# Kernel optimization log

Hardware: AMD Instinct MI355X
Metric: run time of the kernel (lower is better)

The kernel has to match this reference:

```python
import jax, jax.numpy as jnp
import numpy as np

EMBED_DIM = 4096
N_HEADS = 32
N_KV_HEADS = N_HEADS // 2
HEAD_DIM = EMBED_DIM // N_HEADS
MAX_SEQ_LEN = 4096


def setup_inputs() -> dict:
    key = jax.random.key(0)
    k1, k2, k3, k4, k5 = jax.random.split(key, 5)
    b, s = 1, 2048
    x = jax.random.normal(k1, (b, s, EMBED_DIM), dtype=jnp.float32)
    # rotary frequencies: theta=10000, angles[t, i] = t * 10000^{-2i/head_dim}
    inv_freq = 1.0 / (10000.0 ** (np.arange(0, HEAD_DIM, 2, dtype=np.float32) / HEAD_DIM))
    t = np.arange(MAX_SEQ_LEN, dtype=np.float32)
    ang = np.outer(t, inv_freq)  # [max_seq, head_dim/2]
    freqs_cis = jnp.asarray(np.stack([np.cos(ang), np.sin(ang)], axis=-1))  # [max_seq, hd/2, 2]
    scale = 0.02
    wq = jax.random.normal(k2, (EMBED_DIM, EMBED_DIM), dtype=jnp.float32) * scale
    wk = jax.random.normal(k3, (EMBED_DIM, N_KV_HEADS * HEAD_DIM), dtype=jnp.float32) * scale
    wv = jax.random.normal(k4, (EMBED_DIM, N_KV_HEADS * HEAD_DIM), dtype=jnp.float32) * scale
    wo = jax.random.normal(k5, (EMBED_DIM, EMBED_DIM), dtype=jnp.float32) * scale
    return {"x": x, "freqs_cis": freqs_cis, "wq": wq, "wk": wk, "wv": wv, "wo": wo, "start_pos": 0}


def _apply_rope(t, cos, sin):
    # t: [b, s, h, hd]; cos/sin: [1, s, 1, hd/2]
    tr = t.reshape(*t.shape[:-1], HEAD_DIM // 2, 2)
    t0, t1 = tr[..., 0], tr[..., 1]
    o0 = t0 * cos - t1 * sin
    o1 = t0 * sin + t1 * cos
    return jnp.stack([o0, o1], axis=-1).reshape(t.shape)


def reference(x, freqs_cis, wq, wk, wv, wo, start_pos):
    b, s, _ = x.shape
    q = (x @ wq).reshape(b, s, N_HEADS, HEAD_DIM)
    k = (x @ wk).reshape(b, s, N_KV_HEADS, HEAD_DIM)
    v = (x @ wv).reshape(b, s, N_KV_HEADS, HEAD_DIM)
    rep = N_HEADS // N_KV_HEADS
    k = jnp.repeat(k, rep, axis=2)  # GQA: expand KV heads (matches repeat_interleave)
    v = jnp.repeat(v, rep, axis=2)
    fc = freqs_cis[start_pos:start_pos + s]  # [s, hd/2, 2]
    cos = fc[None, :, None, :, 0]
    sin = fc[None, :, None, :, 1]
    q = _apply_rope(q, cos, sin)
    k = _apply_rope(k, cos, sin)
    # [b, h, s, hd]
    q = q.transpose(0, 2, 1, 3)
    k = k.transpose(0, 2, 1, 3)
    v = v.transpose(0, 2, 1, 3)
    scale = 1.0 / jnp.sqrt(jnp.float32(HEAD_DIM))
    scores = jnp.einsum("bhqd,bhkd->bhqk", q, k) * scale
    causal = jnp.tril(jnp.ones((s, s), dtype=bool))
    scores = jnp.where(causal[None, None], scores, jnp.finfo(scores.dtype).min)
    probs = jax.nn.softmax(scores, axis=-1)
    out = jnp.einsum("bhqk,bhkd->bhqd", probs, v)
    out = out.transpose(0, 2, 1, 3).reshape(b, s, EMBED_DIM)
    return out @ wo
```

## Files before the change

### kernel.cpp

```cpp
#include <hip/hip_runtime.h>
#include <stdint.h>

typedef unsigned short u16;
typedef __bf16 bf16x8 __attribute__((ext_vector_type(8)));
typedef float f32x4 __attribute__((ext_vector_type(4)));

#define SEQ   2048
#define EMBED 4096
#define KDIM  4096
#define NH    32
#define NKV   16
#define HD    128
#define KVW   2048

__device__ __forceinline__ float bf2f(u16 u) {
  union { uint32_t u; float f; } v; v.u = ((uint32_t)u) << 16; return v.f;
}
__device__ __forceinline__ u16 f2bf(float f) {
  union { float f; uint32_t u; } v; v.f = f;
  return (u16)((v.u + 0x7FFFu + ((v.u >> 16) & 1u)) >> 16);
}
__device__ __forceinline__ void g2l16(const u16* g, u16* l) {
  __builtin_amdgcn_global_load_lds(
      (const __attribute__((address_space(1))) uint32_t*)g,
      (__attribute__((address_space(3))) uint32_t*)l, 16, 0, 0);
}

__global__ __launch_bounds__(256) void convert_x(
    const float* __restrict__ X, u16* __restrict__ Xb, int nquad) {
  for (int i = blockIdx.x * 256 + threadIdx.x; i < nquad;
       i += gridDim.x * 256) {
    float4 v = *(const float4*)(X + (size_t)i * 4);
    ushort4 o;
    o.x = f2bf(v.x); o.y = f2bf(v.y); o.z = f2bf(v.z); o.w = f2bf(v.w);
    *(ushort4*)(Xb + (size_t)i * 4) = o;
  }
}

__global__ __launch_bounds__(256) void transpose_cvt(
    const float* __restrict__ W, u16* __restrict__ Wt, int K, int N) {
  __shared__ u16 tile[64][68];
  const int t = threadIdx.x;
  const int n0 = blockIdx.x * 64, k0 = blockIdx.y * 64;
#pragma unroll
  for (int i = 0; i < 4; i++) {
    int c = i * 256 + t;
    int r = c >> 4, cq = c & 15;
    float4 v = *(const float4*)(W + (size_t)(k0 + r) * N + n0 + cq * 4);
    tile[r][cq * 4 + 0] = f2bf(v.x); tile[r][cq * 4 + 1] = f2bf(v.y);
    tile[r][cq * 4 + 2] = f2bf(v.z); tile[r][cq * 4 + 3] = f2bf(v.w);
  }
  __syncthreads();
#pragma unroll
  for (int i = 0; i < 4; i++) {
    int c = i * 256 + t;
    int rn = c >> 4, cq = c & 15;
    ushort4 v;
    v.x = tile[cq * 4 + 0][rn];
    v.y = tile[cq * 4 + 1][rn];
    v.z = tile[cq * 4 + 2][rn];
    v.w = tile[cq * 4 + 3][rn];
    *(ushort4*)(Wt + (size_t)(n0 + rn) * K + k0 + cq * 4) = v;
  }
}

__global__ __launch_bounds__(512, 2) void gemm8_qkv(
    const u16* __restrict__ A,
    const u16* __restrict__ B0, const u16* __restrict__ B1,
    const u16* __restrict__ B2,
    u16* __restrict__ Qo, u16* __restrict__ Ko, u16* __restrict__ Vt) {
  __shared__ __align__(16) u16 As[2][256 * 64];
  __shared__ __align__(16) u16 Bs[2][256 * 64];
  const int t = threadIdx.x;
  const int lane = t & 63;
  const int w = t >> 6;
  const int wr = w >> 2;
  const int wc = w & 3;
  const int g = lane >> 4;
  const int l15 = lane & 15;

  const int bid = blockIdx.x;
  const int swz = (bid & 7) * 32 + (bid >> 3);
  const int mb = swz & 7;
  const int nb = swz >> 3;
  const int m0 = mb * 256;

  const u16* Bt; int nrow0;
  if (nb < 16)      { Bt = B0; nrow0 = nb * 256; }
  else if (nb < 24) { Bt = B1; nrow0 = (nb - 16) * 256; }
  else              { Bt = B2; nrow0 = (nb - 24) * 256; }

  auto stageA = [&](int buf, int kt, int h) {
#pragma unroll
    for (int i = 0; i < 2; i++) {
      int c = i * 512 + t;
      int row = c >> 3, sp = c & 7;
      int col = (sp ^ (row & 7)) << 3;
      g2l16(A + (size_t)(m0 + h * 128 + row) * KDIM + kt + col,
            &As[buf][h * 8192 + c * 8]);
    }
  };
  auto stageB = [&](int buf, int kt, int h) {
#pragma unroll
    for (int i = 0; i < 2; i++) {
      int c = i * 512 + t;
      int row = c >> 3, sp = c & 7;
      int col = (sp ^ (row & 7)) << 3;
      g2l16(Bt + (size_t)(nrow0 + h * 128 + row) * KDIM + kt + col,
            &Bs[buf][h * 8192 + c * 8]);
    }
  };

  f32x4 acc[8][4];
#pragma unroll
  for (int i = 0; i < 8; i++)
#pragma unroll
    for (int j = 0; j < 4; j++) acc[i][j] = (f32x4){0.f, 0.f, 0.f, 0.f};

  stageA(0, 0, 0); stageA(0, 0, 1);
  stageB(0, 0, 0); stageB(0, 0, 1);
  stageA(1, 64, 0); stageA(1, 64, 1);
  stageB(1, 64, 0); stageB(1, 64, 1);
  asm volatile("s_waitcnt vmcnt(8)" ::: "memory");
  __builtin_amdgcn_s_barrier();

  const int NT = KDIM / 64;
  for (int ti = 0; ti < NT; ++ti) {
    const int cur = ti & 1;
    const u16* Asc = As[cur];
    const u16* Bsc = Bs[cur];
    const int ktn2 = (ti + 2) * 64;
    bf16x8 a0[2][4], a1[2][4], b0[2][2], b1[2][2];

#pragma unroll
    for (int kk = 0; kk < 2; kk++)
#pragma unroll
      for (int mi = 0; mi < 4; mi++) {
        int r = wr * 128 + mi * 16 + l15;
        int slot = (kk * 4 + g) ^ (r & 7);
        a0[kk][mi] = *(const bf16x8*)(Asc + r * 64 + slot * 8);
      }
#pragma unroll
    for (int kk = 0; kk < 2; kk++)
#pragma unroll
      for (int ni = 0; ni < 2; ni++) {
        int r = wc * 64 + ni * 16 + l15;
        int slot = (kk * 4 + g) ^ (r & 7);
        b0[kk][ni] = *(const bf16x8*)(Bsc + r * 64 + slot * 8);
      }
    __builtin_amdgcn_s_barrier();
    asm volatile("s_waitcnt lgkmcnt(0)" ::: "memory");
    __builtin_amdgcn_sched_barrier(0);
    __builtin_amdgcn_s_setprio(1);
#pragma unroll
    for (int mi = 0; mi < 4; mi++)
#pragma unroll
      for (int ni = 0; ni < 2; ni++)
#pragma unroll
        for (int kk = 0; kk < 2; kk++)
          acc[mi][ni] = __builtin_amdgcn_mfma_f32_16x16x32_bf16(
              a0[kk][mi], b0[kk][ni], acc[mi][ni], 0, 0, 0);
    __builtin_amdgcn_s_setprio(0);
    __builtin_amdgcn_s_barrier();

#pragma unroll
    for (int kk = 0; kk < 2; kk++)
#pragma unroll
      for (int mi = 0; mi < 4; mi++) {
        int r = wr * 128 + 64 + mi * 16 + l15;
        int slot = (kk * 4 + g) ^ (r & 7);
        a1[kk][mi] = *(const bf16x8*)(Asc + r * 64 + slot * 8);
      }
    __builtin_amdgcn_s_barrier();
    asm volatile("s_waitcnt lgkmcnt(0)" ::: "memory");
    __builtin_amdgcn_sched_barrier(0);
    __builtin_amdgcn_s_setprio(1);
#pragma unroll
    for (int mi = 0; mi < 4; mi++)
#pragma unroll
      for (int ni = 0; ni < 2; ni++)
#pragma unroll
        for (int kk = 0; kk < 2; kk++)
          acc[mi + 4][ni] = __builtin_amdgcn_mfma_f32_16x16x32_bf16(
              a1[kk][mi], b0[kk][ni], acc[mi + 4][ni], 0, 0, 0);
    __builtin_amdgcn_s_setprio(0);
    __builtin_amdgcn_s_barrier();

#pragma unroll
    for (int kk = 0; kk < 2; kk++)
#pragma unroll
      for (int ni = 0; ni < 2; ni++) {
        int r = wc * 64 + (ni + 2) * 16 + l15;
        int slot = (kk * 4 + g) ^ (r & 7);
        b1[kk][ni] = *(const bf16x8*)(Bsc + r * 64 + slot * 8);
      }
    if (ti + 2 < NT) { stageA(cur, ktn2, 0); stageA(cur, ktn2, 1); }
    __builtin_amdgcn_s_barrier();
    asm volatile("s_waitcnt lgkmcnt(0)" ::: "memory");
    __builtin_amdgcn_sched_barrier(0);
    __builtin_amdgcn_s_setprio(1);
#pragma unroll
    for (int mi = 0; mi < 4; mi++)
#pragma unroll
      for (int ni = 0; ni < 2; ni++)
#pragma unroll
        for (int kk = 0; kk < 2; kk++)
          acc[mi + 4][ni + 2] = __builtin_amdgcn_mfma_f32_16x16x32_bf16(
              a1[kk][mi], b1[kk][ni], acc[mi + 4][ni + 2], 0, 0, 0);
    __builtin_amdgcn_s_setprio(0);
    __builtin_amdgcn_s_barrier();

    if (ti + 2 < NT) { stageB(cur, ktn2, 0); stageB(cur, ktn2, 1); }
    __builtin_amdgcn_s_barrier();
    __builtin_amdgcn_s_setprio(1);
#pragma unroll
    for (int mi = 0; mi < 4; mi++)
#pragma unroll
      for (int ni = 0; ni < 2; ni++)
#pragma unroll
        for (int kk = 0; kk < 2; kk++)
          acc[mi][ni + 2] = __builtin_amdgcn_mfma_f32_16x16x32_bf16(
              a0[kk][mi], b1[kk][ni], acc[mi][ni + 2], 0, 0, 0);
    __builtin_amdgcn_s_setprio(0);
    if (ti + 2 < NT)      asm volatile("s_waitcnt vmcnt(8)" ::: "memory");
    else if (ti + 1 < NT) asm volatile("s_waitcnt vmcnt(0)" ::: "memory");
    __builtin_amdgcn_s_barrier();
  }

#pragma unroll
  for (int mi = 0; mi < 8; mi++) {
#pragma unroll
    for (int ni = 0; ni < 4; ni++) {
      int rowg = m0 + wr * 128 + mi * 16 + g * 4;
      int ncol = nb * 256 + wc * 64 + ni * 16 + l15;
      if (nb < 16) {
#pragma unroll
        for (int r = 0; r < 4; r++)
          Qo[(size_t)(rowg + r) * EMBED + ncol] = f2bf(acc[mi][ni][r]);
      } else if (nb < 24) {
        int nc = ncol - 4096;
#pragma unroll
        for (int r = 0; r < 4; r++)
          Ko[(size_t)(rowg + r) * KVW + nc] = f2bf(acc[mi][ni][r]);
      } else {
        int nc = ncol - 6144;
        ushort4 v;
        v.x = f2bf(acc[mi][ni][0]); v.y = f2bf(acc[mi][ni][1]);
        v.z = f2bf(acc[mi][ni][2]); v.w = f2bf(acc[mi][ni][3]);
        *(ushort4*)(Vt + (size_t)nc * SEQ + rowg) = v;
      }
    }
  }
}

__global__ __launch_bounds__(512, 2) void gemm8_op(
    const u16* __restrict__ A, const u16* __restrict__ Bt,
    float* __restrict__ Cf) {
  __shared__ __align__(16) u16 As[2][128 * 64];
  __shared__ __align__(16) u16 Bs[2][256 * 64];
  const int t = threadIdx.x;
  const int lane = t & 63;
  const int w = t >> 6;
  const int wr = w >> 2;
  const int wc = w & 3;
  const int g = lane >> 4;
  const int l15 = lane & 15;

  const int bid = blockIdx.x;
  const int swz = (bid & 7) * 32 + (bid >> 3);
  const int mb = swz & 15;
  const int nb = swz >> 4;
  const int m0 = mb * 128;
  const int nrow0 = nb * 256;

  auto stageA = [&](int buf, int kt) {
#pragma unroll
    for (int i = 0; i < 2; i++) {
      int c = i * 512 + t;
      int row = c >> 3, sp = c & 7;
      int col = (sp ^ (row & 7)) << 3;
      g2l16(A + (size_t)(m0 + row) * KDIM + kt + col, &As[buf][c * 8]);
    }
  };
  auto stageB = [&](int buf, int kt) {
#pragma unroll
    for (int i = 0; i < 4; i++) {
      int c = i * 512 + t;
      int row = c >> 3, sp = c & 7;
      int col = (sp ^ (row & 7)) << 3;
      g2l16(Bt + (size_t)(nrow0 + row) * KDIM + kt + col, &Bs[buf][c * 8]);
    }
  };

  f32x4 acc[4][4];
#pragma unroll
  for (int i = 0; i < 4; i++)
#pragma unroll
    for (int j = 0; j < 4; j++) acc[i][j] = (f32x4){0.f, 0.f, 0.f, 0.f};

  stageA(0, 0); stageB(0, 0);
  stageA(1, 64); stageB(1, 64);
  asm volatile("s_waitcnt vmcnt(6)" ::: "memory");
  __builtin_amdgcn_s_barrier();

  const int NT = KDIM / 64;
  for (int ti = 0; ti < NT; ++ti) {
    const int cur = ti & 1;
    const u16* Asc = As[cur];
    const u16* Bsc = Bs[cur];
    const int ktn2 = (ti + 2) * 64;
    bf16x8 a[2][4], b0[2][2], b1[2][2];

#pragma unroll
    for (int kk = 0; kk < 2; kk++)
#pragma unroll
      for (int mi = 0; mi < 4; mi++) {
        int r = wr * 64 + mi * 16 + l15;
        int slot = (kk * 4 + g) ^ (r & 7);
        a[kk][mi] = *(const bf16x8*)(Asc + r * 64 + slot * 8);
      }
#pragma unroll
    for (int kk = 0; kk < 2; kk++)
#pragma unroll
      for (int ni = 0; ni < 2; ni++) {
        int r = wc * 64 + ni * 16 + l15;
        int slot = (kk * 4 + g) ^ (r & 7);
        b0[kk][ni] = *(const bf16x8*)(Bsc + r * 64 + slot * 8);
      }
#pragma unroll
    for (int kk = 0; kk < 2; kk++)
#pragma unroll
      for (int ni = 0; ni < 2; ni++) {
        int r = wc * 64 + (ni + 2) * 16 + l15;
        int slot = (kk * 4 + g) ^ (r & 7);
        b1[kk][ni] = *(const bf16x8*)(Bsc + r * 64 + slot * 8);
      }
    __builtin_amdgcn_s_barrier();
    asm volatile("s_waitcnt lgkmcnt(0)" ::: "memory");
    __builtin_amdgcn_sched_barrier(0);
    __builtin_amdgcn_s_setprio(1);
#pragma unroll
    for (int mi = 0; mi < 4; mi++)
#pragma unroll
      for (int ni = 0; ni < 2; ni++)
#pragma unroll
        for (int kk = 0; kk < 2; kk++)
          acc[mi][ni] = __builtin_amdgcn_mfma_f32_16x16x32_bf16(
              a[kk][mi], b0[kk][ni], acc[mi][ni], 0, 0, 0);
    __builtin_amdgcn_s_setprio(0);
    __builtin_amdgcn_s_barrier();

    if (ti + 2 < NT) { stageA(cur, ktn2); stageB(cur, ktn2); }
    __builtin_amdgcn_s_barrier();
    __builtin_amdgcn_s_setprio(1);
#pragma unroll
    for (int mi = 0; mi < 4; mi++)
#pragma unroll
      for (int ni = 0; ni < 2; ni++)
#pragma unroll
        for (int kk = 0; kk < 2; kk++)
          acc[mi][ni + 2] = __builtin_amdgcn_mfma_f32_16x16x32_bf16(
              a[kk][mi], b1[kk][ni], acc[mi][ni + 2], 0, 0, 0);
    __builtin_amdgcn_s_setprio(0);
    if (ti + 2 < NT)      asm volatile("s_waitcnt vmcnt(6)" ::: "memory");
    else if (ti + 1 < NT) asm volatile("s_waitcnt vmcnt(0)" ::: "memory");
    __builtin_amdgcn_s_barrier();
  }

#pragma unroll
  for (int mi = 0; mi < 4; mi++)
#pragma unroll
    for (int ni = 0; ni < 4; ni++) {
      int rowg = m0 + wr * 64 + mi * 16 + g * 4;
      int ncol = nb * 256 + wc * 64 + ni * 16 + l15;
#pragma unroll
      for (int r = 0; r < 4; r++)
        Cf[(size_t)(rowg + r) * 4096 + ncol] = acc[mi][ni][r];
    }
}

__global__ __launch_bounds__(256) void rope_kernel(
    u16* __restrict__ Q, u16* __restrict__ Kb,
    const float* __restrict__ freqs, const int* __restrict__ start_pos) {
  const int sp = start_pos[0];
  const float qscale = 0.08838834764831845f;
  const int total_q = SEQ * EMBED / 2;
  const int total_k = SEQ * KVW / 2;
  const int total = total_q + total_k;
  for (int idx = blockIdx.x * 256 + threadIdx.x; idx < total;
       idx += gridDim.x * 256) {
    u16* buf; int row, pi; bool isq = idx < total_q;
    if (isq) { row = idx >> 11; pi = idx & 2047; buf = Q + (size_t)row * EMBED; }
    else { int j = idx - total_q; row = j >> 10; pi = j & 1023; buf = Kb + (size_t)row * KVW; }
    int i = pi & 63;
    float2 cs = *(const float2*)(freqs + (size_t)(sp + row) * 128 + i * 2);
    float c = cs.x, s = cs.y;
    ushort2 tv = *(ushort2*)(buf + pi * 2);
    float t0 = bf2f(tv.x), t1 = bf2f(tv.y);
    float o0 = t0 * c - t1 * s;
    float o1 = t0 * s + t1 * c;
    if (isq) { o0 *= qscale; o1 *= qscale; }
    ushort2 o; o.x = f2bf(o0); o.y = f2bf(o1);
    *(ushort2*)(buf + pi * 2) = o;
  }
}

__global__ __launch_bounds__(256, 4) void attn_kernel(
    const u16* __restrict__ Q, const u16* __restrict__ Kb,
    const u16* __restrict__ Vt, u16* __restrict__ O) {
  __shared__ __align__(16) u16 KV[16384];
  __shared__ u16 Ps[4][16 * 72];

  const int t = threadIdx.x;
  const int lane = t & 63;
  const int w = t >> 6;
  const int g = lane >> 4;
  const int l15 = lane & 15;
  const int bid = blockIdx.x;
  const int qb = 31 - (bid >> 5);
  const int h = bid & 31;
  const int hk = h >> 1;

  auto stageK = [&](int kv) {
#pragma unroll
    for (int i = 0; i < 4; i++) {
      int c = i * 256 + t;
      int row = c >> 4, spp = c & 15;
      int col = ((spp ^ (row & 7)) << 3);
      g2l16(Kb + (size_t)(kv * 64 + row) * KVW + hk * HD + col, &KV[c * 8]);
    }
  };
  auto stageV = [&](int kv) {
#pragma unroll
    for (int i = 0; i < 4; i++) {
      int c = i * 256 + t;
      int row = c >> 3, spp = c & 7;
      int col = ((spp ^ (row & 7)) << 3);
      g2l16(Vt + (size_t)(hk * HD + row) * SEQ + kv * 64 + col,
            &KV[8192 + c * 8]);
    }
  };

#pragma unroll
  for (int i = 0; i < 4; i++) {
    int c = i * 256 + t;
    int row = c >> 4, spp = c & 15;
    int col = ((spp ^ (row & 7)) << 3);
    g2l16(Q + (size_t)(qb * 64 + row) * EMBED + h * HD + col, &KV[c * 8]);
  }
  asm volatile("s_waitcnt vmcnt(0)" ::: "memory");
  __builtin_amdgcn_s_barrier();

  bf16x8 qf[4];
  {
    int r = w * 16 + l15;
#pragma unroll
    for (int kk = 0; kk < 4; kk++) {
      int ps = (kk * 4 + g) ^ (r & 7);
      qf[kk] = *(const bf16x8*)(&KV[r * 128 + ps * 8]);
    }
  }
  asm volatile("s_waitcnt lgkmcnt(0)" ::: "memory");
  __builtin_amdgcn_s_barrier();

  f32x4 oacc[8];
#pragma unroll
  for (int i = 0; i < 8; i++) oacc[i] = (f32x4){0.f, 0.f, 0.f, 0.f};
  float mrow = -1e30f, lrow = 0.f;
  const int qg = qb * 64 + w * 16 + l15;

  for (int kv = 0; kv <= qb; kv++) {
    stageK(kv); stageV(kv);
    asm volatile("s_waitcnt vmcnt(0)" ::: "memory");
    __builtin_amdgcn_s_barrier();

    f32x4 sfragT[4];
    __builtin_amdgcn_s_setprio(1);
#pragma unroll
    for (int ni = 0; ni < 4; ni++) {
      f32x4 s = (f32x4){0.f, 0.f, 0.f, 0.f};
      int r = ni * 16 + l15;
#pragma unroll
      for (int kk = 0; kk < 4; kk++) {
        int ps = (kk * 4 + g) ^ (r & 7);
        bf16x8 a = *(const bf16x8*)(&KV[r * 128 + ps * 8]);
        s = __builtin_amdgcn_mfma_f32_16x16x32_bf16(a, qf[kk], s, 0, 0, 0);
      }
      sfragT[ni] = s;
    }
    __builtin_amdgcn_s_setprio(0);

    if (kv == qb) {
#pragma unroll
      for (int ni = 0; ni < 4; ni++) {
        int colg = kv * 64 + ni * 16 + g * 4;
#pragma unroll
        for (int r = 0; r < 4; r++)
          if (colg + r > qg) sfragT[ni][r] = -1e30f;
      }
    }

    float m16 = sfragT[0][0];
#pragma unroll
    for (int ni = 0; ni < 4; ni++)
#pragma unroll
      for (int r = 0; r < 4; r++) m16 = fmaxf(m16, sfragT[ni][r]);
    m16 = fmaxf(m16, __shfl_xor(m16, 16));
    m16 = fmaxf(m16, __shfl_xor(m16, 32));
    float mnew = fmaxf(mrow, m16);
    float sc = __expf(mrow - mnew);
    mrow = mnew;

    float rsum = 0.f;
#pragma unroll
    for (int ni = 0; ni < 4; ni++) {
#pragma unroll
      for (int r = 0; r < 4; r++) {
        float p = __expf(sfragT[ni][r] - mrow);
        rsum += p;
        Ps[w][l15 * 72 + ni * 16 + g * 4 + r] = f2bf(p);
      }
    }
    rsum += __shfl_xor(rsum, 16);
    rsum += __shfl_xor(rsum, 32);
    lrow = lrow * sc + rsum;

    float scr[4];
#pragma unroll
    for (int r = 0; r < 4; r++) scr[r] = __shfl(sc, g * 4 + r, 64);
#pragma unroll
    for (int nf = 0; nf < 8; nf++)
#pragma unroll
      for (int r = 0; r < 4; r++) oacc[nf][r] *= scr[r];

    asm volatile("s_waitcnt lgkmcnt(0)" ::: "memory");

    bf16x8 pa[2];
#pragma unroll
    for (int kk = 0; kk < 2; kk++)
      pa[kk] = *(const bf16x8*)(&Ps[w][l15 * 72 + kk * 32 + g * 8]);
    __builtin_amdgcn_s_setprio(1);
#pragma unroll
    for (int nf = 0; nf < 8; nf++) {
      int r = nf * 16 + l15;
#pragma unroll
      for (int kk = 0; kk < 2; kk++) {
        int ps = (kk * 4 + g) ^ (r & 7);
        bf16x8 b = *(const bf16x8*)(&KV[8192 + r * 64 + ps * 8]);
        oacc[nf] = __builtin_amdgcn_mfma_f32_16x16x32_bf16(pa[kk], b, oacc[nf], 0, 0, 0);
      }
    }
    __builtin_amdgcn_s_setprio(0);
    __builtin_amdgcn_s_barrier();
  }

  float lr[4];
#pragma unroll
  for (int r = 0; r < 4; r++) lr[r] = __shfl(lrow, g * 4 + r, 64);
#pragma unroll
  for (int nf = 0; nf < 8; nf++) {
#pragma unroll
    for (int r = 0; r < 4; r++) {
      int rowg = qb * 64 + w * 16 + g * 4 + r;
      float v = oacc[nf][r] / lr[r];
      O[(size_t)rowg * EMBED + h * HD + nf * 16 + l15] = f2bf(v);
    }
  }
}

extern "C" void kernel_launch(void* const* d_in, const int* in_sizes, int n_in,
                              void* d_out, int out_size, void* d_ws, size_t ws_size,
                              hipStream_t stream) {
  const float* x  = (const float*)d_in[0];
  const float* fc = (const float*)d_in[1];
  const float* wq = (const float*)d_in[2];
  const float* wk = (const float*)d_in[3];
  const float* wv = (const float*)d_in[4];
  const float* wo = (const float*)d_in[5];
  const int* sp = (const int*)d_in[6];

  char* ws = (char*)d_ws;
  u16* wqT = (u16*)(ws);
  u16* wkT = (u16*)(ws + 33554432ull);
  u16* wvT = (u16*)(ws + 50331648ull);
  u16* woT = (u16*)(ws + 67108864ull);
  u16* xb  = (u16*)(ws + 100663296ull);
  u16* Qb  = (u16*)(ws + 117440512ull);
  u16* Kb  = (u16*)(ws + 134217728ull);
  u16* Vt  = (u16*)(ws + 142606336ull);
  u16* Ob  = (u16*)(ws + 150994944ull);

  convert_x<<<dim3(2048), 256, 0, stream>>>(x, xb, SEQ * EMBED / 4);
  transpose_cvt<<<dim3(64, 64), 256, 0, stream>>>(wq, wqT, 4096, 4096);
  transpose_cvt<<<dim3(32, 64), 256, 0, stream>>>(wk, wkT, 4096, 2048);
  transpose_cvt<<<dim3(32, 64), 256, 0, stream>>>(wv, wvT, 4096, 2048);
  transpose_cvt<<<dim3(64, 64), 256, 0, stream>>>(wo, woT, 4096, 4096);

  gemm8_qkv<<<dim3(256), 512, 0, stream>>>(xb, wqT, wkT, wvT, Qb, Kb, Vt);
  rope_kernel<<<dim3(2048), 256, 0, stream>>>(Qb, Kb, fc, sp);
  attn_kernel<<<dim3(1024), 256, 0, stream>>>(Qb, Kb, Vt, Ob);
  gemm8_op<<<dim3(256), 512, 0, stream>>>(Ob, woT, (float*)d_out);
}
```

Baseline: 360.5 us.

## Software-pipeline LDS fragment reads across k-tiles in QKV and output GEMMs

Restructures the main loops of both GEMM kernels so the first A/B fragments for the next k-tile are read from LDS while MFMAs of the current tile run, with ping-pong register sets and a loop unrolled by two. It removes several barriers and lgkmcnt waits per iteration and interleaves global-to-LDS staging with fragment reads and MFMA blocks. This should hide LDS latency and cut sync overhead. In exchange it raises register pressure and relies on tighter vmcnt counts for correctness.

```diff
diff --git a/kernel.cpp b/kernel.cpp
--- a/kernel.cpp
+++ b/kernel.cpp
@@ -24,6 +24,11 @@
   __builtin_amdgcn_global_load_lds(
       (const __attribute__((address_space(1))) uint32_t*)g,
       (__attribute__((address_space(3))) uint32_t*)l, 16, 0, 0);
+}
+__device__ __forceinline__ void BAR() {
+  asm volatile("" ::: "memory");
+  __builtin_amdgcn_s_barrier();
+  asm volatile("" ::: "memory");
 }
 
 __global__ __launch_bounds__(256) void convert_x(
@@ -78,6 +83,7 @@
   const int wc = w & 3;
   const int g = lane >> 4;
   const int l15 = lane & 15;
+  const int NT = KDIM / 64;
 
   const int bid = blockIdx.x;
   const int swz = (bid & 7) * 32 + (bid >> 3);
@@ -90,7 +96,7 @@
   else if (nb < 24) { Bt = B1; nrow0 = (nb - 16) * 256; }
   else              { Bt = B2; nrow0 = (nb - 24) * 256; }
 
-  auto stageA = [&](int buf, int kt, int h) {
+  auto stA = [&](int buf, int kt, int h) {
 #pragma unroll
     for (int i = 0; i < 2; i++) {
       int c = i * 512 + t;
@@ -100,7 +106,7 @@
             &As[buf][h * 8192 + c * 8]);
     }
   };
-  auto stageB = [&](int buf, int kt, int h) {
+  auto stB = [&](int buf, int kt, int h) {
 #pragma unroll
     for (int i = 0; i < 2; i++) {
       int c = i * 512 + t;
@@ -117,114 +123,97 @@
 #pragma unroll
     for (int j = 0; j < 4; j++) acc[i][j] = (f32x4){0.f, 0.f, 0.f, 0.f};
 
-  stageA(0, 0, 0); stageA(0, 0, 1);
-  stageB(0, 0, 0); stageB(0, 0, 1);
-  stageA(1, 64, 0); stageA(1, 64, 1);
-  stageB(1, 64, 0); stageB(1, 64, 1);
-  asm volatile("s_waitcnt vmcnt(8)" ::: "memory");
-  __builtin_amdgcn_s_barrier();
-
-  const int NT = KDIM / 64;
-  for (int ti = 0; ti < NT; ++ti) {
-    const int cur = ti & 1;
-    const u16* Asc = As[cur];
-    const u16* Bsc = Bs[cur];
-    const int ktn2 = (ti + 2) * 64;
-    bf16x8 a0[2][4], a1[2][4], b0[2][2], b1[2][2];
-
+  auto rdA0 = [&](const u16* S, bf16x8 (&d)[2][4]) {
 #pragma unroll
     for (int kk = 0; kk < 2; kk++)
 #pragma unroll
       for (int mi = 0; mi < 4; mi++) {
         int r = wr * 128 + mi * 16 + l15;
-        int slot = (kk * 4 + g) ^ (r & 7);
-        a0[kk][mi] = *(const bf16x8*)(Asc + r * 64 + slot * 8);
-      }
+        int sl = (kk * 4 + g) ^ (r & 7);
+        d[kk][mi] = *(const bf16x8*)(S + r * 64 + sl * 8);
+      }
+  };
+  auto rdA1 = [&](const u16* S, bf16x8 (&d)[2][4]) {
+#pragma unroll
+    for (int kk = 0; kk < 2; kk++)
+#pragma unroll
+      for (int mi = 0; mi < 4; mi++) {
+        int r = wr * 128 + 64 + mi * 16 + l15;
+        int sl = (kk * 4 + g) ^ (r & 7);
+        d[kk][mi] = *(const bf16x8*)(S + r * 64 + sl * 8);
+      }
+  };
+  auto rdB0 = [&](const u16* S, bf16x8 (&d)[2][2]) {
 #pragma unroll
     for (int kk = 0; kk < 2; kk++)
 #pragma unroll
       for (int ni = 0; ni < 2; ni++) {
         int r = wc * 64 + ni * 16 + l15;
-        int slot = (kk * 4 + g) ^ (r & 7);
-        b0[kk][ni] = *(const bf16x8*)(Bsc + r * 64 + slot * 8);
-      }
-    __builtin_amdgcn_s_barrier();
-    asm volatile("s_waitcnt lgkmcnt(0)" ::: "memory");
-    __builtin_amdgcn_sched_barrier(0);
-    __builtin_amdgcn_s_setprio(1);
-#pragma unroll
-    for (int mi = 0; mi < 4; mi++)
-#pragma unroll
-      for (int ni = 0; ni < 2; ni++)
-#pragma unroll
-        for (int kk = 0; kk < 2; kk++)
-          acc[mi][ni] = __builtin_amdgcn_mfma_f32_16x16x32_bf16(
-              a0[kk][mi], b0[kk][ni], acc[mi][ni], 0, 0, 0);
-    __builtin_amdgcn_s_setprio(0);
-    __builtin_amdgcn_s_barrier();
-
-#pragma unroll
-    for (int kk = 0; kk < 2; kk++)
-#pragma unroll
-      for (int mi = 0; mi < 4; mi++) {
-        int r = wr * 128 + 64 + mi * 16 + l15;
-        int slot = (kk * 4 + g) ^ (r & 7);
-        a1[kk][mi] = *(const bf16x8*)(Asc + r * 64 + slot * 8);
-      }
-    __builtin_amdgcn_s_barrier();
-    asm volatile("s_waitcnt lgkmcnt(0)" ::: "memory");
-    __builtin_amdgcn_sched_barrier(0);
-    __builtin_amdgcn_s_setprio(1);
-#pragma unroll
-    for (int mi = 0; mi < 4; mi++)
-#pragma unroll
-      for (int ni = 0; ni < 2; ni++)
-#pragma unroll
-        for (int kk = 0; kk < 2; kk++)
-          acc[mi + 4][ni] = __builtin_amdgcn_mfma_f32_16x16x32_bf16(
-              a1[kk][mi], b0[kk][ni], acc[mi + 4][ni], 0, 0, 0);
-    __builtin_amdgcn_s_setprio(0);
-    __builtin_amdgcn_s_barrier();
-
+        int sl = (kk * 4 + g) ^ (r & 7);
+        d[kk][ni] = *(const bf16x8*)(S + r * 64 + sl * 8);
+      }
+  };
+  auto rdB1 = [&](const u16* S, bf16x8 (&d)[2][2]) {
 #pragma unroll
     for (int kk = 0; kk < 2; kk++)
 #pragma unroll
       for (int ni = 0; ni < 2; ni++) {
         int r = wc * 64 + (ni + 2) * 16 + l15;
-        int slot = (kk * 4 + g) ^ (r & 7);
-        b1[kk][ni] = *(const bf16x8*)(Bsc + r * 64 + slot * 8);
-      }
-    if (ti + 2 < NT) { stageA(cur, ktn2, 0); stageA(cur, ktn2, 1); }
-    __builtin_amdgcn_s_barrier();
-    asm volatile("s_waitcnt lgkmcnt(0)" ::: "memory");
+        int sl = (kk * 4 + g) ^ (r & 7);
+        d[kk][ni] = *(const bf16x8*)(S + r * 64 + sl * 8);
+      }
+  };
+  auto mmQ = [&](bf16x8 (&Af)[2][4], bf16x8 (&Bf)[2][2], int mo, int no) {
+    __builtin_amdgcn_s_setprio(1);
+#pragma unroll
+    for (int mi = 0; mi < 4; mi++)
+#pragma unroll
+      for (int ni = 0; ni < 2; ni++)
+#pragma unroll
+        for (int kk = 0; kk < 2; kk++)
+          acc[mi + mo][ni + no] = __builtin_amdgcn_mfma_f32_16x16x32_bf16(
+              Af[kk][mi], Bf[kk][ni], acc[mi + mo][ni + no], 0, 0, 0);
+    __builtin_amdgcn_s_setprio(0);
+  };
+
+  stA(0, 0, 0); stA(0, 0, 1); stB(0, 0, 0); stB(0, 0, 1);
+  stA(1, 64, 0); stA(1, 64, 1); stB(1, 64, 0); stB(1, 64, 1);
+  asm volatile("s_waitcnt vmcnt(8)" ::: "memory");
+  BAR();
+
+  bf16x8 a0X[2][4], b0X[2][2], a0Y[2][4], b0Y[2][2];
+  rdA0(As[0], a0X); rdB0(Bs[0], b0X);
+
+  auto body = [&](int ti, const u16* CA, const u16* CB,
+                  const u16* NA, const u16* NB,
+                  bf16x8 (&a0)[2][4], bf16x8 (&b0)[2][2],
+                  bf16x8 (&a0n)[2][4], bf16x8 (&b0n)[2][2], int sb) {
+    bf16x8 a1[2][4], b1[2][2];
+    const int kt2 = (ti + 2) * 64;
+    rdA1(CA, a1);
     __builtin_amdgcn_sched_barrier(0);
-    __builtin_amdgcn_s_setprio(1);
-#pragma unroll
-    for (int mi = 0; mi < 4; mi++)
-#pragma unroll
-      for (int ni = 0; ni < 2; ni++)
-#pragma unroll
-        for (int kk = 0; kk < 2; kk++)
-          acc[mi + 4][ni + 2] = __builtin_amdgcn_mfma_f32_16x16x32_bf16(
-              a1[kk][mi], b1[kk][ni], acc[mi + 4][ni + 2], 0, 0, 0);
-    __builtin_amdgcn_s_setprio(0);
-    __builtin_amdgcn_s_barrier();
-
-    if (ti + 2 < NT) { stageB(cur, ktn2, 0); stageB(cur, ktn2, 1); }
-    __builtin_amdgcn_s_barrier();
-    __builtin_amdgcn_s_setprio(1);
-#pragma unroll
-    for (int mi = 0; mi < 4; mi++)
-#pragma unroll
-      for (int ni = 0; ni < 2; ni++)
-#pragma unroll
-        for (int kk = 0; kk < 2; kk++)
-          acc[mi][ni + 2] = __builtin_amdgcn_mfma_f32_16x16x32_bf16(
-              a0[kk][mi], b1[kk][ni], acc[mi][ni + 2], 0, 0, 0);
-    __builtin_amdgcn_s_setprio(0);
-    if (ti + 2 < NT)      asm volatile("s_waitcnt vmcnt(8)" ::: "memory");
-    else if (ti + 1 < NT) asm volatile("s_waitcnt vmcnt(0)" ::: "memory");
-    __builtin_amdgcn_s_barrier();
+    mmQ(a0, b0, 0, 0);
+    rdB1(CB, b1);
+    __builtin_amdgcn_sched_barrier(0);
+    mmQ(a1, b0, 4, 0);
+    asm volatile("s_waitcnt vmcnt(4)" ::: "memory");
+    BAR();
+    if (ti + 2 < NT) { stA(sb, kt2, 0); stA(sb, kt2, 1); }
+    if (ti + 1 < NT) rdA0(NA, a0n);
+    __builtin_amdgcn_sched_barrier(0);
+    mmQ(a1, b1, 4, 2);
+    if (ti + 2 < NT) asm volatile("s_waitcnt vmcnt(4)" ::: "memory");
+    else             asm volatile("s_waitcnt vmcnt(0)" ::: "memory");
+    BAR();
+    if (ti + 2 < NT) { stB(sb, kt2, 0); stB(sb, kt2, 1); }
+    if (ti + 1 < NT) rdB0(NB, b0n);
+    __builtin_amdgcn_sched_barrier(0);
+    mmQ(a0, b1, 0, 2);
+  };
+
+  for (int ti = 0; ti < NT; ti += 2) {
+    body(ti,     As[0], Bs[0], As[1], Bs[1], a0X, b0X, a0Y, b0Y, 0);
+    body(ti + 1, As[1], Bs[1], As[0], Bs[0], a0Y, b0Y, a0X, b0X, 1);
   }
 
 #pragma unroll
@@ -265,6 +254,7 @@
   const int wc = w & 3;
   const int g = lane >> 4;
   const int l15 = lane & 15;
+  const int NT = KDIM / 64;
 
   const int bid = blockIdx.x;
   const int swz = (bid & 7) * 32 + (bid >> 3);
@@ -273,7 +263,9 @@
   const int m0 = mb * 128;
   const int nrow0 = nb * 256;
 
-  auto stageA = [&](int buf, int kt) {
+  auto stA = [&](int buf, int kt) {
+#pragma unroll
+    for (int i = 0; i < 1; i++) { }
 #pragma unroll
     for (int i = 0; i < 2; i++) {
       int c = i * 512 + t;
@@ -282,7 +274,7 @@
       g2l16(A + (size_t)(m0 + row) * KDIM + kt + col, &As[buf][c * 8]);
     }
   };
-  auto stageB = [&](int buf, int kt) {
+  auto stB = [&](int buf, int kt) {
 #pragma unroll
     for (int i = 0; i < 4; i++) {
       int c = i * 512 + t;
@@ -298,73 +290,81 @@
 #pragma unroll
     for (int j = 0; j < 4; j++) acc[i][j] = (f32x4){0.f, 0.f, 0.f, 0.f};
 
-  stageA(0, 0); stageB(0, 0);
-  stageA(1, 64); stageB(1, 64);
-  asm volatile("s_waitcnt vmcnt(6)" ::: "memory");
-  __builtin_amdgcn_s_barrier();
-
-  const int NT = KDIM / 64;
-  for (int ti = 0; ti < NT; ++ti) {
-    const int cur = ti & 1;
-    const u16* Asc = As[cur];
-    const u16* Bsc = Bs[cur];
-    const int ktn2 = (ti + 2) * 64;
-    bf16x8 a[2][4], b0[2][2], b1[2][2];
-
+  auto rdA = [&](const u16* S, bf16x8 (&d)[2][4]) {
 #pragma unroll
     for (int kk = 0; kk < 2; kk++)
 #pragma unroll
       for (int mi = 0; mi < 4; mi++) {
         int r = wr * 64 + mi * 16 + l15;
-        int slot = (kk * 4 + g) ^ (r & 7);
-        a[kk][mi] = *(const bf16x8*)(Asc + r * 64 + slot * 8);
-      }
+        int sl = (kk * 4 + g) ^ (r & 7);
+        d[kk][mi] = *(const bf16x8*)(S + r * 64 + sl * 8);
+      }
+  };
+  auto rdB0 = [&](const u16* S, bf16x8 (&d)[2][2]) {
 #pragma unroll
     for (int kk = 0; kk < 2; kk++)
 #pragma unroll
       for (int ni = 0; ni < 2; ni++) {
         int r = wc * 64 + ni * 16 + l15;
-        int slot = (kk * 4 + g) ^ (r & 7);
-        b0[kk][ni] = *(const bf16x8*)(Bsc + r * 64 + slot * 8);
-      }
+        int sl = (kk * 4 + g) ^ (r & 7);
+        d[kk][ni] = *(const bf16x8*)(S + r * 64 + sl * 8);
+      }
+  };
+  auto rdB1 = [&](const u16* S, bf16x8 (&d)[2][2]) {
 #pragma unroll
     for (int kk = 0; kk < 2; kk++)
 #pragma unroll
       for (int ni = 0; ni < 2; ni++) {
         int r = wc * 64 + (ni + 2) * 16 + l15;
-        int slot = (kk * 4 + g) ^ (r & 7);
-        b1[kk][ni] = *(const bf16x8*)(Bsc + r * 64 + slot * 8);
-      }
-    __builtin_amdgcn_s_barrier();
-    asm volatile("s_waitcnt lgkmcnt(0)" ::: "memory");
+        int sl = (kk * 4 + g) ^ (r & 7);
+        d[kk][ni] = *(const bf16x8*)(S + r * 64 + sl * 8);
+      }
+  };
+  auto mmQ = [&](bf16x8 (&Af)[2][4], bf16x8 (&Bf)[2][2], int no) {
+    __builtin_amdgcn_s_setprio(1);
+#pragma unroll
+    for (int mi = 0; mi < 4; mi++)
+#pragma unroll
+      for (int ni = 0; ni < 2; ni++)
+#pragma unroll
+        for (int kk = 0; kk < 2; kk++)
+          acc[mi][ni + no] = __builtin_amdgcn_mfma_f32_16x16x32_bf16(
+              Af[kk][mi], Bf[kk][ni], acc[mi][ni + no], 0, 0, 0);
+    __builtin_amdgcn_s_setprio(0);
+  };
+
+  stA(0, 0); stB(0, 0);
+  stA(1, 64); stB(1, 64);
+  asm volatile("s_waitcnt vmcnt(6)" ::: "memory");
+  BAR();
+
+  bf16x8 aX[2][4], b0X[2][2], aY[2][4], b0Y[2][2];
+  rdA(As[0], aX); rdB0(Bs[0], b0X);
+
+  auto body = [&](int ti, const u16* CB, const u16* NA, const u16* NB,
+                  bf16x8 (&a)[2][4], bf16x8 (&b0)[2][2],
+                  bf16x8 (&an)[2][4], bf16x8 (&b0n)[2][2], int sb) {
+    bf16x8 b1[2][2];
+    const int kt2 = (ti + 2) * 64;
+    rdB1(CB, b1);
     __builtin_amdgcn_sched_barrier(0);
-    __builtin_amdgcn_s_setprio(1);
-#pragma unroll
-    for (int mi = 0; mi < 4; mi++)
-#pragma unroll
-      for (int ni = 0; ni < 2; ni++)
-#pragma unroll
-        for (int kk = 0; kk < 2; kk++)
-          acc[mi][ni] = __builtin_amdgcn_mfma_f32_16x16x32_bf16(
-              a[kk][mi], b0[kk][ni], acc[mi][ni], 0, 0, 0);
-    __builtin_amdgcn_s_setprio(0);
-    __builtin_amdgcn_s_barrier();
-
-    if (ti + 2 < NT) { stageA(cur, ktn2); stageB(cur, ktn2); }
-    __builtin_amdgcn_s_barrier();
-    __builtin_amdgcn_s_setprio(1);
-#pragma unroll
-    for (int mi = 0; mi < 4; mi++)
-#pragma unroll
-      for (int ni = 0; ni < 2; ni++)
-#pragma unroll
-        for (int kk = 0; kk < 2; kk++)
-          acc[mi][ni + 2] = __builtin_amdgcn_mfma_f32_16x16x32_bf16(
-              a[kk][mi], b1[kk][ni], acc[mi][ni + 2], 0, 0, 0);
-    __builtin_amdgcn_s_setprio(0);
-    if (ti + 2 < NT)      asm volatile("s_waitcnt vmcnt(6)" ::: "memory");
-    else if (ti + 1 < NT) asm volatile("s_waitcnt vmcnt(0)" ::: "memory");
-    __builtin_amdgcn_s_barrier();
+    mmQ(a, b0, 0);
+    asm volatile("s_waitcnt vmcnt(4)" ::: "memory");
+    BAR();
+    if (ti + 2 < NT) stA(sb, kt2);
+    if (ti + 1 < NT) rdA(NA, an);
+    __builtin_amdgcn_sched_barrier(0);
+    mmQ(a, b1, 2);
+    if (ti + 2 < NT) asm volatile("s_waitcnt vmcnt(2)" ::: "memory");
+    else             asm volatile("s_waitcnt vmcnt(0)" ::: "memory");
+    BAR();
+    if (ti + 2 < NT) stB(sb, kt2);
+    if (ti + 1 < NT) rdB0(NB, b0n);
+  };
+
+  for (int ti = 0; ti < NT; ti += 2) {
+    body(ti,     Bs[0], As[1], Bs[1], aX, b0X, aY, b0Y, 0);
+    body(ti + 1, Bs[1], As[0], Bs[0], aY, b0Y, aX, b0X, 1);
   }
 
 #pragma unroll
```

New measurement: 796.9 us. 121% more time.

## Share KV tiles across GQA head pairs and simplify QKV GEMM pipeline

Applied to the files above, without the earlier changes.

The attention kernel now has each block process both query heads that share one KV head, so each K/V tile loaded into LDS feeds two heads. This halves the grid and doubles per-thread accumulator state, and launch bounds drop to 2 blocks per CU. The QKV GEMM is restructured from an interleaved, multi-barrier schedule with prefetch distance 2 into a simple double buffer with one barrier per iteration that loads all fragments up front. It also lowers its occupancy hint to 1, which raises register pressure and may expose more global-load latency.

```diff
diff --git a/kernel.cpp b/kernel.cpp
--- a/kernel.cpp
+++ b/kernel.cpp
@@ -24,6 +24,11 @@
   __builtin_amdgcn_global_load_lds(
       (const __attribute__((address_space(1))) uint32_t*)g,
       (__attribute__((address_space(3))) uint32_t*)l, 16, 0, 0);
+}
+__device__ __forceinline__ void BAR() {
+  asm volatile("" ::: "memory");
+  __builtin_amdgcn_s_barrier();
+  asm volatile("" ::: "memory");
 }
 
 __global__ __launch_bounds__(256) void convert_x(
@@ -64,7 +69,7 @@
   }
 }
 
-__global__ __launch_bounds__(512, 2) void gemm8_qkv(
+__global__ __launch_bounds__(512, 1) void gemm8_qkv(
     const u16* __restrict__ A,
     const u16* __restrict__ B0, const u16* __restrict__ B1,
     const u16* __restrict__ B2,
@@ -78,6 +83,7 @@
   const int wc = w & 3;
   const int g = lane >> 4;
   const int l15 = lane & 15;
+  const int NT = KDIM / 64;
 
   const int bid = blockIdx.x;
   const int swz = (bid & 7) * 32 + (bid >> 3);
@@ -90,7 +96,7 @@
   else if (nb < 24) { Bt = B1; nrow0 = (nb - 16) * 256; }
   else              { Bt = B2; nrow0 = (nb - 24) * 256; }
 
-  auto stageA = [&](int buf, int kt, int h) {
+  auto stA = [&](int buf, int kt, int h) {
 #pragma unroll
     for (int i = 0; i < 2; i++) {
       int c = i * 512 + t;
@@ -100,7 +106,7 @@
             &As[buf][h * 8192 + c * 8]);
     }
   };
-  auto stageB = [&](int buf, int kt, int h) {
+  auto stB = [&](int buf, int kt, int h) {
 #pragma unroll
     for (int i = 0; i < 2; i++) {
       int c = i * 512 + t;
@@ -117,114 +123,62 @@
 #pragma unroll
     for (int j = 0; j < 4; j++) acc[i][j] = (f32x4){0.f, 0.f, 0.f, 0.f};
 
-  stageA(0, 0, 0); stageA(0, 0, 1);
-  stageB(0, 0, 0); stageB(0, 0, 1);
-  stageA(1, 64, 0); stageA(1, 64, 1);
-  stageB(1, 64, 0); stageB(1, 64, 1);
-  asm volatile("s_waitcnt vmcnt(8)" ::: "memory");
-  __builtin_amdgcn_s_barrier();
-
-  const int NT = KDIM / 64;
+  auto mmQ = [&](bf16x8 (&Af)[2][4], bf16x8 (&Bf)[2][2], int mo, int no) {
+    __builtin_amdgcn_s_setprio(1);
+#pragma unroll
+    for (int mi = 0; mi < 4; mi++)
+#pragma unroll
+      for (int ni = 0; ni < 2; ni++)
+#pragma unroll
+        for (int kk = 0; kk < 2; kk++)
+          acc[mi + mo][ni + no] = __builtin_amdgcn_mfma_f32_16x16x32_bf16(
+              Af[kk][mi], Bf[kk][ni], acc[mi + mo][ni + no], 0, 0, 0);
+    __builtin_amdgcn_s_setprio(0);
+  };
+
+  stA(0, 0, 0); stA(0, 0, 1); stB(0, 0, 0); stB(0, 0, 1);
+
   for (int ti = 0; ti < NT; ++ti) {
     const int cur = ti & 1;
     const u16* Asc = As[cur];
     const u16* Bsc = Bs[cur];
-    const int ktn2 = (ti + 2) * 64;
+    const int kt1 = (ti + 1) * 64;
+
+    asm volatile("s_waitcnt vmcnt(0)" ::: "memory");
+    BAR();
+    if (ti + 1 < NT) {
+      stA(cur ^ 1, kt1, 0); stA(cur ^ 1, kt1, 1);
+      stB(cur ^ 1, kt1, 0); stB(cur ^ 1, kt1, 1);
+    }
     bf16x8 a0[2][4], a1[2][4], b0[2][2], b1[2][2];
-
 #pragma unroll
     for (int kk = 0; kk < 2; kk++)
 #pragma unroll
       for (int mi = 0; mi < 4; mi++) {
-        int r = wr * 128 + mi * 16 + l15;
-        int slot = (kk * 4 + g) ^ (r & 7);
-        a0[kk][mi] = *(const bf16x8*)(Asc + r * 64 + slot * 8);
+        int r0 = wr * 128 + mi * 16 + l15;
+        int s0 = (kk * 4 + g) ^ (r0 & 7);
+        a0[kk][mi] = *(const bf16x8*)(Asc + r0 * 64 + s0 * 8);
+        int r1 = r0 + 64;
+        int s1 = (kk * 4 + g) ^ (r1 & 7);
+        a1[kk][mi] = *(const bf16x8*)(Asc + r1 * 64 + s1 * 8);
       }
 #pragma unroll
     for (int kk = 0; kk < 2; kk++)
 #pragma unroll
       for (int ni = 0; ni < 2; ni++) {
-        int r = wc * 64 + ni * 16 + l15;
-        int slot = (kk * 4 + g) ^ (r & 7);
-        b0[kk][ni] = *(const bf16x8*)(Bsc + r * 64 + slot * 8);
-      }
-    __builtin_amdgcn_s_barrier();
+        int r0 = wc * 64 + ni * 16 + l15;
+        int s0 = (kk * 4 + g) ^ (r0 & 7);
+        b0[kk][ni] = *(const bf16x8*)(Bsc + r0 * 64 + s0 * 8);
+        int r1 = wc * 64 + (ni + 2) * 16 + l15;
+        int s1 = (kk * 4 + g) ^ (r1 & 7);
+        b1[kk][ni] = *(const bf16x8*)(Bsc + r1 * 64 + s1 * 8);
+      }
     asm volatile("s_waitcnt lgkmcnt(0)" ::: "memory");
     __builtin_amdgcn_sched_barrier(0);
-    __builtin_amdgcn_s_setprio(1);
-#pragma unroll
-    for (int mi = 0; mi < 4; mi++)
-#pragma unroll
-      for (int ni = 0; ni < 2; ni++)
-#pragma unroll
-        for (int kk = 0; kk < 2; kk++)
-          acc[mi][ni] = __builtin_amdgcn_mfma_f32_16x16x32_bf16(
-              a0[kk][mi], b0[kk][ni], acc[mi][ni], 0, 0, 0);
-    __builtin_amdgcn_s_setprio(0);
-    __builtin_amdgcn_s_barrier();
-
-#pragma unroll
-    for (int kk = 0; kk < 2; kk++)
-#pragma unroll
-      for (int mi = 0; mi < 4; mi++) {
-        int r = wr * 128 + 64 + mi * 16 + l15;
-        int slot = (kk * 4 + g) ^ (r & 7);
-        a1[kk][mi] = *(const bf16x8*)(Asc + r * 64 + slot * 8);
-      }
-    __builtin_amdgcn_s_barrier();
-    asm volatile("s_waitcnt lgkmcnt(0)" ::: "memory");
-    __builtin_amdgcn_sched_barrier(0);
-    __builtin_amdgcn_s_setprio(1);
-#pragma unroll
-    for (int mi = 0; mi < 4; mi++)
-#pragma unroll
-      for (int ni = 0; ni < 2; ni++)
-#pragma unroll
-        for (int kk = 0; kk < 2; kk++)
-          acc[mi + 4][ni] = __builtin_amdgcn_mfma_f32_16x16x32_bf16(
-              a1[kk][mi], b0[kk][ni], acc[mi + 4][ni], 0, 0, 0);
-    __builtin_amdgcn_s_setprio(0);
-    __builtin_amdgcn_s_barrier();
-
-#pragma unroll
-    for (int kk = 0; kk < 2; kk++)
-#pragma unroll
-      for (int ni = 0; ni < 2; ni++) {
-        int r = wc * 64 + (ni + 2) * 16 + l15;
-        int slot = (kk * 4 + g) ^ (r & 7);
-        b1[kk][ni] = *(const bf16x8*)(Bsc + r * 64 + slot * 8);
-      }
-    if (ti + 2 < NT) { stageA(cur, ktn2, 0); stageA(cur, ktn2, 1); }
-    __builtin_amdgcn_s_barrier();
-    asm volatile("s_waitcnt lgkmcnt(0)" ::: "memory");
-    __builtin_amdgcn_sched_barrier(0);
-    __builtin_amdgcn_s_setprio(1);
-#pragma unroll
-    for (int mi = 0; mi < 4; mi++)
-#pragma unroll
-      for (int ni = 0; ni < 2; ni++)
-#pragma unroll
-        for (int kk = 0; kk < 2; kk++)
-          acc[mi + 4][ni + 2] = __builtin_amdgcn_mfma_f32_16x16x32_bf16(
-              a1[kk][mi], b1[kk][ni], acc[mi + 4][ni + 2], 0, 0, 0);
-    __builtin_amdgcn_s_setprio(0);
-    __builtin_amdgcn_s_barrier();
-
-    if (ti + 2 < NT) { stageB(cur, ktn2, 0); stageB(cur, ktn2, 1); }
-    __builtin_amdgcn_s_barrier();
-    __builtin_amdgcn_s_setprio(1);
-#pragma unroll
-    for (int mi = 0; mi < 4; mi++)
-#pragma unroll
-      for (int ni = 0; ni < 2; ni++)
-#pragma unroll
-        for (int kk = 0; kk < 2; kk++)
-          acc[mi][ni + 2] = __builtin_amdgcn_mfma_f32_16x16x32_bf16(
-              a0[kk][mi], b1[kk][ni], acc[mi][ni + 2], 0, 0, 0);
-    __builtin_amdgcn_s_setprio(0);
-    if (ti + 2 < NT)      asm volatile("s_waitcnt vmcnt(8)" ::: "memory");
-    else if (ti + 1 < NT) asm volatile("s_waitcnt vmcnt(0)" ::: "memory");
-    __builtin_amdgcn_s_barrier();
+    mmQ(a0, b0, 0, 0);
+    mmQ(a1, b0, 4, 0);
+    mmQ(a1, b1, 4, 2);
+    mmQ(a0, b1, 0, 2);
   }
 
 #pragma unroll
@@ -405,7 +359,7 @@
   }
 }
 
-__global__ __launch_bounds__(256, 4) void attn_kernel(
+__global__ __launch_bounds__(256, 2) void attn_kernel(
     const u16* __restrict__ Q, const u16* __restrict__ Kb,
     const u16* __restrict__ Vt, u16* __restrict__ O) {
   __shared__ __align__(16) u16 KV[16384];
@@ -417,9 +371,9 @@
   const int g = lane >> 4;
   const int l15 = lane & 15;
   const int bid = blockIdx.x;
-  const int qb = 31 - (bid >> 5);
-  const int h = bid & 31;
-  const int hk = h >> 1;
+  const int qb = 31 - (bid >> 4);
+  const int hk = bid & 15;
+  const int hA = hk * 2, hB = hk * 2 + 1;
 
   auto stageK = [&](int kv) {
 #pragma unroll
@@ -446,27 +400,33 @@
     int c = i * 256 + t;
     int row = c >> 4, spp = c & 15;
     int col = ((spp ^ (row & 7)) << 3);
-    g2l16(Q + (size_t)(qb * 64 + row) * EMBED + h * HD + col, &KV[c * 8]);
+    g2l16(Q + (size_t)(qb * 64 + row) * EMBED + hA * HD + col, &KV[c * 8]);
+    g2l16(Q + (size_t)(qb * 64 + row) * EMBED + hB * HD + col,
+          &KV[8192 + c * 8]);
   }
   asm volatile("s_waitcnt vmcnt(0)" ::: "memory");
   __builtin_amdgcn_s_barrier();
 
-  bf16x8 qf[4];
+  bf16x8 qfA[4], qfB[4];
   {
     int r = w * 16 + l15;
 #pragma unroll
     for (int kk = 0; kk < 4; kk++) {
       int ps = (kk * 4 + g) ^ (r & 7);
-      qf[kk] = *(const bf16x8*)(&KV[r * 128 + ps * 8]);
+      qfA[kk] = *(const bf16x8*)(&KV[r * 128 + ps * 8]);
+      qfB[kk] = *(const bf16x8*)(&KV[8192 + r * 128 + ps * 8]);
     }
   }
   asm volatile("s_waitcnt lgkmcnt(0)" ::: "memory");
   __builtin_amdgcn_s_barrier();
 
-  f32x4 oacc[8];
-#pragma unroll
-  for (int i = 0; i < 8; i++) oacc[i] = (f32x4){0.f, 0.f, 0.f, 0.f};
-  float mrow = -1e30f, lrow = 0.f;
+  f32x4 oA[8], oB[8];
+#pragma unroll
+  for (int i = 0; i < 8; i++) {
+    oA[i] = (f32x4){0.f, 0.f, 0.f, 0.f};
+    oB[i] = (f32x4){0.f, 0.f, 0.f, 0.f};
+  }
+  float mA = -1e30f, lA = 0.f, mB = -1e30f, lB = 0.f;
   const int qg = qb * 64 + w * 16 + l15;
 
   for (int kv = 0; kv <= qb; kv++) {
@@ -474,19 +434,21 @@
     asm volatile("s_waitcnt vmcnt(0)" ::: "memory");
     __builtin_amdgcn_s_barrier();
 
-    f32x4 sfragT[4];
+    f32x4 sA[4], sB[4];
     __builtin_amdgcn_s_setprio(1);
 #pragma unroll
     for (int ni = 0; ni < 4; ni++) {
-      f32x4 s = (f32x4){0.f, 0.f, 0.f, 0.f};
+      f32x4 xA = (f32x4){0.f, 0.f, 0.f, 0.f};
+      f32x4 xB = (f32x4){0.f, 0.f, 0.f, 0.f};
       int r = ni * 16 + l15;
 #pragma unroll
       for (int kk = 0; kk < 4; kk++) {
         int ps = (kk * 4 + g) ^ (r & 7);
         bf16x8 a = *(const bf16x8*)(&KV[r * 128 + ps * 8]);
-        s = __builtin_amdgcn_mfma_f32_16x16x32_bf16(a, qf[kk], s, 0, 0, 0);
-      }
-      sfragT[ni] = s;
+        xA = __builtin_amdgcn_mfma_f32_16x16x32_bf16(a, qfA[kk], xA, 0, 0, 0);
+        xB = __builtin_amdgcn_mfma_f32_16x16x32_bf16(a, qfB[kk], xB, 0, 0, 0);
+      }
+      sA[ni] = xA; sB[ni] = xB;
     }
     __builtin_amdgcn_s_setprio(0);
 
@@ -496,49 +458,83 @@
         int colg = kv * 64 + ni * 16 + g * 4;
 #pragma unroll
         for (int r = 0; r < 4; r++)
-          if (colg + r > qg) sfragT[ni][r] = -1e30f;
-      }
-    }
-
-    float m16 = sfragT[0][0];
-#pragma unroll
-    for (int ni = 0; ni < 4; ni++)
-#pragma unroll
-      for (int r = 0; r < 4; r++) m16 = fmaxf(m16, sfragT[ni][r]);
-    m16 = fmaxf(m16, __shfl_xor(m16, 16));
-    m16 = fmaxf(m16, __shfl_xor(m16, 32));
-    float mnew = fmaxf(mrow, m16);
-    float sc = __expf(mrow - mnew);
-    mrow = mnew;
-
-    float rsum = 0.f;
-#pragma unroll
-    for (int ni = 0; ni < 4; ni++) {
-#pragma unroll
-      for (int r = 0; r < 4; r++) {
-        float p = __expf(sfragT[ni][r] - mrow);
-        rsum += p;
-        Ps[w][l15 * 72 + ni * 16 + g * 4 + r] = f2bf(p);
-      }
-    }
-    rsum += __shfl_xor(rsum, 16);
-    rsum += __shfl_xor(rsum, 32);
-    lrow = lrow * sc + rsum;
-
-    float scr[4];
-#pragma unroll
-    for (int r = 0; r < 4; r++) scr[r] = __shfl(sc, g * 4 + r, 64);
-#pragma unroll
-    for (int nf = 0; nf < 8; nf++)
-#pragma unroll
-      for (int r = 0; r < 4; r++) oacc[nf][r] *= scr[r];
-
-    asm volatile("s_waitcnt lgkmcnt(0)" ::: "memory");
-
-    bf16x8 pa[2];
-#pragma unroll
-    for (int kk = 0; kk < 2; kk++)
-      pa[kk] = *(const bf16x8*)(&Ps[w][l15 * 72 + kk * 32 + g * 8]);
+          if (colg + r > qg) { sA[ni][r] = -1e30f; sB[ni][r] = -1e30f; }
+      }
+    }
+
+    bf16x8 paA[2], paB[2];
+    {
+      float m16 = sA[0][0];
+#pragma unroll
+      for (int ni = 0; ni < 4; ni++)
+#pragma unroll
+        for (int r = 0; r < 4; r++) m16 = fmaxf(m16, sA[ni][r]);
+      m16 = fmaxf(m16, __shfl_xor(m16, 16));
+      m16 = fmaxf(m16, __shfl_xor(m16, 32));
+      float mnew = fmaxf(mA, m16);
+      float sc = __expf(mA - mnew);
+      mA = mnew;
+      float rsum = 0.f;
+#pragma unroll
+      for (int ni = 0; ni < 4; ni++)
+#pragma unroll
+        for (int r = 0; r < 4; r++) {
+          float p = __expf(sA[ni][r] - mA);
+          rsum += p;
+          Ps[w][l15 * 72 + ni * 16 + g * 4 + r] = f2bf(p);
+        }
+      rsum += __shfl_xor(rsum, 16);
+      rsum += __shfl_xor(rsum, 32);
+      lA = lA * sc + rsum;
+      float scr[4];
+#pragma unroll
+      for (int r = 0; r < 4; r++) scr[r] = __shfl(sc, g * 4 + r, 64);
+#pragma unroll
+      for (int nf = 0; nf < 8; nf++)
+#pragma unroll
+        for (int r = 0; r < 4; r++) oA[nf][r] *= scr[r];
+      asm volatile("s_waitcnt lgkmcnt(0)" ::: "memory");
+#pragma unroll
+      for (int kk = 0; kk < 2; kk++)
+        paA[kk] = *(const bf16x8*)(&Ps[w][l15 * 72 + kk * 32 + g * 8]);
+      asm volatile("s_waitcnt lgkmcnt(0)" ::: "memory");
+    }
+    {
+      float m16 = sB[0][0];
+#pragma unroll
+      for (int ni = 0; ni < 4; ni++)
+#pragma unroll
+        for (int r = 0; r < 4; r++) m16 = fmaxf(m16, sB[ni][r]);
+      m16 = fmaxf(m16, __shfl_xor(m16, 16));
+      m16 = fmaxf(m16, __shfl_xor(m16, 32));
+      float mnew = fmaxf(mB, m16);
+      float sc = __expf(mB - mnew);
+      mB = mnew;
+      float rsum = 0.f;
+#pragma unroll
+      for (int ni = 0; ni < 4; ni++)
+#pragma unroll
+        for (int r = 0; r < 4; r++) {
+          float p = __expf(sB[ni][r] - mB);
+          rsum += p;
+          Ps[w][l15 * 72 + ni * 16 + g * 4 + r] = f2bf(p);
+        }
+      rsum += __shfl_xor(rsum, 16);
+      rsum += __shfl_xor(rsum, 32);
+      lB = lB * sc + rsum;
+      float scr[4];
+#pragma unroll
+      for (int r = 0; r < 4; r++) scr[r] = __shfl(sc, g * 4 + r, 64);
+#pragma unroll
+      for (int nf = 0; nf < 8; nf++)
+#pragma unroll
+        for (int r = 0; r < 4; r++) oB[nf][r] *= scr[r];
+      asm volatile("s_waitcnt lgkmcnt(0)" ::: "memory");
+#pragma unroll
+      for (int kk = 0; kk < 2; kk++)
+        paB[kk] = *(const bf16x8*)(&Ps[w][l15 * 72 + kk * 32 + g * 8]);
+    }
+
     __builtin_amdgcn_s_setprio(1);
 #pragma unroll
     for (int nf = 0; nf < 8; nf++) {
@@ -547,23 +543,27 @@
       for (int kk = 0; kk < 2; kk++) {
         int ps = (kk * 4 + g) ^ (r & 7);
         bf16x8 b = *(const bf16x8*)(&KV[8192 + r * 64 + ps * 8]);
-        oacc[nf] = __builtin_amdgcn_mfma_f32_16x16x32_bf16(pa[kk], b, oacc[nf], 0, 0, 0);
+        oA[nf] = __builtin_amdgcn_mfma_f32_16x16x32_bf16(paA[kk], b, oA[nf], 0, 0, 0);
+        oB[nf] = __builtin_amdgcn_mfma_f32_16x16x32_bf16(paB[kk], b, oB[nf], 0, 0, 0);
       }
     }
     __builtin_amdgcn_s_setprio(0);
     __builtin_amdgcn_s_barrier();
   }
 
-  float lr[4];
-#pragma unroll
-  for (int r = 0; r < 4; r++) lr[r] = __shfl(lrow, g * 4 + r, 64);
+  float lrA[4], lrB[4];
+#pragma unroll
+  for (int r = 0; r < 4; r++) {
+    lrA[r] = __shfl(lA, g * 4 + r, 64);
+    lrB[r] = __shfl(lB, g * 4 + r, 64);
+  }
 #pragma unroll
   for (int nf = 0; nf < 8; nf++) {
 #pragma unroll
     for (int r = 0; r < 4; r++) {
       int rowg = qb * 64 + w * 16 + g * 4 + r;
-      float v = oacc[nf][r] / lr[r];
-      O[(size_t)rowg * EMBED + h * HD + nf * 16 + l15] = f2bf(v);
+      O[(size_t)rowg * EMBED + hA * HD + nf * 16 + l15] = f2bf(oA[nf][r] / lrA[r]);
+      O[(size_t)rowg * EMBED + hB * HD + nf * 16 + l15] = f2bf(oB[nf][r] / lrB[r]);
     }
   }
 }
@@ -598,6 +598,6 @@
 
   gemm8_qkv<<<dim3(256), 512, 0, stream>>>(xb, wqT, wkT, wvT, Qb, Kb, Vt);
   rope_kernel<<<dim3(2048), 256, 0, stream>>>(Qb, Kb, fc, sp);
-  attn_kernel<<<dim3(1024), 256, 0, stream>>>(Qb, Kb, Vt, Ob);
+  attn_kernel<<<dim3(512), 256, 0, stream>>>(Qb, Kb, Vt, Ob);
   gemm8_op<<<dim3(256), 512, 0, stream>>>(Ob, woT, (float*)d_out);
 }
```

Measured after the change: 386.2 us. 7.1% more time.
